# Performance work log

Hardware: AMD Instinct MI355X
Metric: run time of the kernel (lower is better)

## Reference

```python
import jax, jax.numpy as jnp
import numpy as np

B, R, N, F = 16, 13, 392, 256
POOL_CH = 512
NB_CLASSES = 200
ALPHA = 0.5
BN_EPS = 1e-3


def gcn_norm_ones(n):
    # GCNConv.preprocess on an all-ones adjacency: A_hat = A + I, D = (n+1)I,
    # D^-1/2 A_hat D^-1/2 = (ones + eye) / (n + 1)
    return (jnp.ones((n, n), jnp.float32) + jnp.eye(n, dtype=jnp.float32)) / (n + 1.0)


def appnp(x, A, w, b, alpha):
    # Spektral APPNPConv, no hidden layers, mlp_activation='sigmoid', propagations=1
    h = jax.nn.sigmoid(x @ w + b)
    return (1.0 - alpha) * jnp.einsum('mn,...nf->...mf', A, h) + alpha * h


def gat_dense(x, A, kernel, attn_s, attn_n, bias):
    # Faithful translation of the modified GATConv._call_dense
    xk = jnp.einsum('...ni,iho->...nho', x, kernel)            # [..., N, H, Fo]
    s = jnp.einsum('...nhi,iho->...nho', xk, attn_s)           # [..., N, H, 1]
    nb = jnp.einsum('...nhi,iho->...nho', xk, attn_n)          # [..., N, H, 1]
    nb = jnp.einsum('...abc->...cba', nb)                      # [..., 1, H, N]
    coef = jax.nn.leaky_relu(s + nb, 0.2)                      # [..., N, H, N]
    # add_self_loops then mask where a == 0 (normalized ones adjacency -> no masking)
    a = A.at[jnp.arange(A.shape[-1]), jnp.arange(A.shape[-1])].set(1.0)
    mask = jnp.where(a == 0.0, -1e10, 0.0).astype(coef.dtype)  # [N, N]
    coef = coef + mask[:, None, :]
    coef = jax.nn.softmax(coef, axis=-1)
    out = jnp.einsum('...nhm,...mhi->...nhi', coef, xk)        # [..., N, H, Fo]
    out = out.reshape(out.shape[:-2] + (-1,)) + bias           # concat heads
    return jax.nn.elu(out)


def setup_inputs() -> dict:
    key = jax.random.key(0)
    ks = jax.random.split(key, 8)
    s = lambda k, shape, sc: (jax.random.normal(k, shape, jnp.float32) * sc)
    return {
        'x': s(ks[0], (B, R, N, F), 1.0),
        'w_mlp': s(ks[1], (F, F), F ** -0.5),
        'b_mlp': jnp.zeros((F,), jnp.float32),
        'k_gat': s(ks[2], (F, 1, F), F ** -0.5),
        'a_self': s(ks[3], (F, 1, 1), F ** -0.5),
        'a_neigh': s(ks[4], (F, 1, 1), F ** -0.5),
        'b_gat': jnp.zeros((F,), jnp.float32),
        'wf_pool': s(ks[5], (F, POOL_CH), F ** -0.5),
        'bf_pool': jnp.zeros((POOL_CH,), jnp.float32),
        'wa_pool': s(ks[6], (F, POOL_CH), F ** -0.5),
        'ba_pool': jnp.zeros((POOL_CH,), jnp.float32),
        'bn_gamma': jnp.ones((POOL_CH,), jnp.float32),
        'bn_beta': jnp.zeros((POOL_CH,), jnp.float32),
        'bn_mean': jnp.zeros((POOL_CH,), jnp.float32),
        'bn_var': jnp.ones((POOL_CH,), jnp.float32),
        'w_out': s(ks[7], (POOL_CH, NB_CLASSES), POOL_CH ** -0.5),
        'b_out': jnp.zeros((NB_CLASSES,), jnp.float32),
    }


def reference(x, w_mlp, b_mlp, k_gat, a_self, a_neigh, b_gat,
              wf_pool, bf_pool, wa_pool, ba_pool,
              bn_gamma, bn_beta, bn_mean, bn_var, w_out, b_out):
    A_intra = gcn_norm_ones(N)   # [N, N]
    A_inter = gcn_norm_ones(R)   # [R, R]

    # Intra-ROI: APPNP + residual, GAT + residual (all R graphs share weights/adj)
    h = appnp(x, A_intra, w_mlp, b_mlp, ALPHA) + x                      # [B,R,N,F]
    x2_intra = gat_dense(h, A_intra, k_gat, a_self, a_neigh, b_gat) + h
    x2_intra = x2_intra.reshape(x.shape[0], R * N, F)

    # Inter-ROI: transpose so ROIs are the graph nodes
    xt = jnp.transpose(x, (0, 2, 1, 3))                                 # [B,N,R,F]
    h2 = appnp(xt, A_inter, w_mlp, b_mlp, ALPHA) + xt
    x2_inter = gat_dense(h2, A_inter, k_gat, a_self, a_neigh, b_gat) + h2
    x2_inter = x2_inter.reshape(x.shape[0], N * R, F)

    x2 = jnp.concatenate([x2_intra, x2_inter], axis=1)                  # [B, 2RN, F]

    # GlobalAttentionPool(512)
    attn = jax.nn.sigmoid(x2 @ wa_pool + ba_pool)
    feat = x2 @ wf_pool + bf_pool
    pooled = jnp.sum(attn * feat, axis=1)                               # [B, 512]

    # BatchNorm (inference) + softmax classifier
    bn = (pooled - bn_mean) * jax.lax.rsqrt(bn_var + BN_EPS) * bn_gamma + bn_beta
    return jax.nn.softmax(bn @ w_out + b_out, axis=-1)
```

## Files before the change

kernel.cpp:

```cpp
#include <hip/hip_runtime.h>
#include <hip/hip_bf16.h>

#define B_    16
#define R_    13
#define N_    392
#define F_    256
#define RN_   (R_*N_)
#define M_    (B_*RN_)
#define POOL_ 512
#define NCLS_ 200
#define KP_   416
#define WPS_  424

typedef __attribute__((ext_vector_type(4))) float f32x4;
typedef __attribute__((ext_vector_type(8))) short bf16x8;
typedef __attribute__((ext_vector_type(8))) unsigned short u16x8;

__device__ __forceinline__ unsigned short f2b(float f){
  union { float f; unsigned u; } v; v.f = f;
  unsigned r = v.u + 0x7FFF + ((v.u >> 16) & 1);
  return (unsigned short)(r >> 16);
}
__device__ __forceinline__ float b2f(unsigned short b){
  union { unsigned u; float f; } v; v.u = ((unsigned)b) << 16;
  return v.f;
}

__device__ __forceinline__ float warpMax(float v){
  #pragma unroll
  for (int o = 32; o; o >>= 1) v = fmaxf(v, __shfl_down(v, o));
  return v;
}
__device__ __forceinline__ float warpSum(float v){
  #pragma unroll
  for (int o = 32; o; o >>= 1) v += __shfl_down(v, o);
  return v;
}
__device__ __forceinline__ float blockMax(float v, float* red){
  v = warpMax(v);
  __syncthreads();
  if ((threadIdx.x & 63) == 0) red[threadIdx.x >> 6] = v;
  __syncthreads();
  return fmaxf(fmaxf(red[0], red[1]), fmaxf(red[2], red[3]));
}
__device__ __forceinline__ float blockSum(float v, float* red){
  v = warpSum(v);
  __syncthreads();
  if ((threadIdx.x & 63) == 0) red[threadIdx.x >> 6] = v;
  __syncthreads();
  return red[0] + red[1] + red[2] + red[3];
}
__device__ __forceinline__ float eluf(float v){
  return v > 0.f ? v : (expf(v) - 1.f);
}

__global__ __launch_bounds__(256) void cvt_wt(const float* __restrict__ W,
    unsigned short* __restrict__ Wt, int K, int N){
  const int id = blockIdx.x*256 + threadIdx.x;
  if (id < K*N){
    const int n = id / K, k = id - n*K;
    Wt[id] = f2b(W[k*N + n]);
  }
}

__global__ __launch_bounds__(256) void cvt_x(const float* __restrict__ x,
    unsigned short* __restrict__ xb){
  const long t = (long)blockIdx.x*256 + threadIdx.x;
  const float4 a = *(const float4*)&x[t*8];
  const float4 b = *(const float4*)&x[t*8 + 4];
  u16x8 o = {f2b(a.x),f2b(a.y),f2b(a.z),f2b(a.w),f2b(b.x),f2b(b.y),f2b(b.z),f2b(b.w)};
  *(u16x8*)&xb[t*8] = o;
}

__global__ __launch_bounds__(256) void cvt_xT(const float* __restrict__ x,
    unsigned short* __restrict__ xb){
  const long t = (long)blockIdx.x*256 + threadIdx.x;
  const int l  = (int)(t >> 5);
  const int c8 = ((int)t & 31) * 8;
  const int b  = l / RN_;
  const int rem = l - b*RN_;
  const int n  = rem / R_;
  const int r  = rem - n*R_;
  const long prow = (long)(b*R_ + r)*N_ + n;
  const float4 a  = *(const float4*)&x[prow*F_ + c8];
  const float4 bb = *(const float4*)&x[prow*F_ + c8 + 4];
  u16x8 o = {f2b(a.x),f2b(a.y),f2b(a.z),f2b(a.w),f2b(bb.x),f2b(bb.y),f2b(bb.z),f2b(bb.w)};
  *(u16x8*)&xb[(long)l*F_ + c8] = o;
}

template<int ACT>
__global__ __launch_bounds__(256) void mfma_gemm(
    const unsigned short* __restrict__ A, const unsigned short* __restrict__ Wt,
    const float* __restrict__ bias, unsigned short* __restrict__ out){
  __shared__ unsigned short A_lds[128][72];
  __shared__ unsigned short W_lds[64][72];
  const int tid = threadIdx.x;
  const int lane = tid & 63, wid = tid >> 6;
  const int wr = wid >> 1, wc = wid & 1;
  const int lr = lane & 15, lk = lane >> 4;
  const int row0 = blockIdx.x * 128;
  const int col0 = blockIdx.y * 64;

  f32x4 acc[4][2] = {};
  for (int k0 = 0; k0 < 256; k0 += 64){
    #pragma unroll
    for (int i = 0; i < 4; ++i){
      const int chunk = tid + i*256;
      const int r = chunk >> 3, c8 = (chunk & 7)*8;
      *(u16x8*)&A_lds[r][c8] = *(const u16x8*)&A[(long)(row0 + r)*F_ + k0 + c8];
    }
    #pragma unroll
    for (int i = 0; i < 2; ++i){
      const int chunk = tid + i*256;
      const int r = chunk >> 3, c8 = (chunk & 7)*8;
      *(u16x8*)&W_lds[r][c8] = *(const u16x8*)&Wt[(long)(col0 + r)*F_ + k0 + c8];
    }
    __syncthreads();
    #pragma unroll
    for (int kk = 0; kk < 64; kk += 32){
      bf16x8 af[4], bf[2];
      #pragma unroll
      for (int m = 0; m < 4; ++m)
        af[m] = *(const bf16x8*)&A_lds[wr*64 + m*16 + lr][kk + lk*8];
      #pragma unroll
      for (int n = 0; n < 2; ++n)
        bf[n] = *(const bf16x8*)&W_lds[wc*32 + n*16 + lr][kk + lk*8];
      #pragma unroll
      for (int m = 0; m < 4; ++m)
        #pragma unroll
        for (int n = 0; n < 2; ++n)
          acc[m][n] = __builtin_amdgcn_mfma_f32_16x16x32_bf16(af[m], bf[n], acc[m][n], 0, 0, 0);
    }
    __syncthreads();
  }
  #pragma unroll
  for (int m = 0; m < 4; ++m){
    const int gr = row0 + wr*64 + m*16 + lk*4;
    #pragma unroll
    for (int n = 0; n < 2; ++n){
      const int gc = col0 + wc*32 + n*16 + lr;
      #pragma unroll
      for (int q = 0; q < 4; ++q){
        float v = acc[m][n][q];
        if (ACT) v = 1.f/(1.f + expf(-(v + bias[gc])));
        out[(long)(gr + q)*F_ + gc] = f2b(v);
      }
    }
  }
}

__global__ __launch_bounds__(256) void xkT_k(const unsigned short* __restrict__ xk,
    unsigned short* __restrict__ xkT){
  __shared__ unsigned short tile[32][36];
  const int n0 = blockIdx.x * 32;
  const int f0 = blockIdx.y * 32;
  const int g  = blockIdx.z;
  const int t  = threadIdx.x;
  {
    const int nl = t >> 3, fl = (t & 7)*4;
    ushort4 v = {0,0,0,0};
    const int n = n0 + nl;
    if (n < N_) v = *(const ushort4*)&xk[((long)g*N_ + n)*F_ + f0 + fl];
    tile[nl][fl] = v.x; tile[nl][fl+1] = v.y; tile[nl][fl+2] = v.z; tile[nl][fl+3] = v.w;
  }
  __syncthreads();
  {
    const int fl = t >> 3, nl = (t & 7)*4;
    ushort4 o = {tile[nl][fl], tile[nl+1][fl], tile[nl+2][fl], tile[nl+3][fl]};
    *(ushort4*)&xkT[((long)g*F_ + f0 + fl)*KP_ + n0 + nl] = o;
  }
}

__global__ __launch_bounds__(256) void colsum_k(const unsigned short* __restrict__ h1,
    float* __restrict__ S, int nn){
  const int g = blockIdx.x;
  const int f = threadIdx.x;
  const unsigned short* base = h1 + (long)g*nn*F_ + f;
  float s = 0.f;
  for (int n = 0; n < nn; ++n) s += b2f(base[(long)n*F_]);
  S[(long)g*F_ + f] = s;
}

template<int XMODE>
__global__ __launch_bounds__(256) void combine_k(const unsigned short* __restrict__ h1,
    const float* __restrict__ S, const float* __restrict__ x,
    unsigned short* __restrict__ hb){
  const long t = (long)blockIdx.x*256 + threadIdx.x;
  const long row = t >> 6;
  const int f4 = ((int)t & 63) * 4;
  int g, xrow;
  if (XMODE == 0){ g = (int)(row / N_); xrow = (int)row; }
  else {
    g = (int)(row / R_);
    const int b   = (int)(row / RN_);
    const int rem = (int)(row - (long)b*RN_);
    const int n   = rem / R_;
    const int r   = rem - n*R_;
    xrow = (b*R_ + r)*N_ + n;
  }
  const float inv = (XMODE == 0) ? (1.f/(N_+1)) : (1.f/(R_+1));
  const ushort4 hraw = *(const ushort4*)&h1[row*F_ + f4];
  const float4 h1v = {b2f(hraw.x), b2f(hraw.y), b2f(hraw.z), b2f(hraw.w)};
  const float4 Sv  = *(const float4*)&S[(long)g*F_ + f4];
  const float4 xv  = *(const float4*)&x[(long)xrow*F_ + f4];
  float4 o;
  o.x = 0.5f*(Sv.x + h1v.x)*inv + 0.5f*h1v.x + xv.x;
  o.y = 0.5f*(Sv.y + h1v.y)*inv + 0.5f*h1v.y + xv.y;
  o.z = 0.5f*(Sv.z + h1v.z)*inv + 0.5f*h1v.z + xv.z;
  o.w = 0.5f*(Sv.w + h1v.w)*inv + 0.5f*h1v.w + xv.w;
  const ushort4 ob = {f2b(o.x), f2b(o.y), f2b(o.z), f2b(o.w)};
  *(ushort4*)&hb[row*F_ + f4] = ob;
}

__global__ __launch_bounds__(256) void st_k(const unsigned short* __restrict__ xk,
    const float* __restrict__ a_self, const float* __restrict__ a_neigh,
    float* __restrict__ sv, float* __restrict__ tv){
  const int lane = threadIdx.x & 63;
  const int wid  = threadIdx.x >> 6;
  const long row = (long)blockIdx.x*4 + wid;
  const ushort4 raw = *(const ushort4*)&xk[row*F_ + lane*4];
  const float4 v  = {b2f(raw.x), b2f(raw.y), b2f(raw.z), b2f(raw.w)};
  const float4 as = *(const float4*)&a_self[lane*4];
  const float4 an = *(const float4*)&a_neigh[lane*4];
  float s = v.x*as.x + v.y*as.y + v.z*as.z + v.w*as.w;
  float t = v.x*an.x + v.y*an.y + v.z*an.z + v.w*an.w;
  #pragma unroll
  for (int o = 32; o; o >>= 1){ s += __shfl_down(s, o); t += __shfl_down(t, o); }
  if (lane == 0){ sv[row] = s; tv[row] = t; }
}

__global__ __launch_bounds__(256) void attn_intra_k(
    const unsigned short* __restrict__ xkT, const float* __restrict__ sv,
    const float* __restrict__ tv, const float* __restrict__ bg,
    unsigned short* __restrict__ hx2){
  __shared__ unsigned short Wp[64][WPS_];
  __shared__ float t_lds[N_];
  __shared__ float s_lds[64];
  __shared__ float invr[64];
  __shared__ float red[4];
  const int g  = blockIdx.y;
  const int m0 = blockIdx.x * 64;
  const int tid = threadIdx.x;
  const int lane = tid & 63, wid = tid >> 6;

  for (int n = tid; n < N_; n += 256) t_lds[n] = tv[(long)g*N_ + n];
  if (tid < 64) s_lds[tid] = (m0 + tid < N_) ? sv[(long)g*N_ + m0 + tid] : 0.f;
  __syncthreads();
  float tl = -1e30f;
  for (int n = tid; n < N_; n += 256) tl = fmaxf(tl, t_lds[n]);
  const float tmax = blockMax(tl, red);

  for (int j = 0; j < 16; ++j){
    const int row = wid*16 + j;
    const float sm = s_lds[row];
    float zm = sm + tmax; zm = zm > 0.f ? zm : 0.2f*zm;
    float loc = 0.f;
    for (int n = lane; n < KP_; n += 64){
      float e = 0.f;
      if (n < N_){
        float z = sm + t_lds[n];
        z = z > 0.f ? z : 0.2f*z;
        e = expf(z - zm);
        loc += e;
      }
      Wp[row][n] = f2b(e);
    }
    loc = warpSum(loc);
    if (lane == 0) invr[row] = 1.f / loc;
  }
  __syncthreads();

  const int lr = lane & 15, lk = lane >> 4;
  const int c0w = wid * 64;
  const unsigned short* xkTg = xkT + (long)g*F_*KP_;
  f32x4 acc[4][4] = {};
  for (int ks = 0; ks < 13; ++ks){
    const int k0 = ks*32;
    bf16x8 af[4], bfr[4];
    #pragma unroll
    for (int mi = 0; mi < 4; ++mi)
      af[mi] = *(const bf16x8*)&Wp[mi*16 + lr][k0 + lk*8];
    #pragma unroll
    for (int ni = 0; ni < 4; ++ni)
      bfr[ni] = *(const bf16x8*)&xkTg[(long)(c0w + ni*16 + lr)*KP_ + k0 + lk*8];
    #pragma unroll
    for (int mi = 0; mi < 4; ++mi)
      #pragma unroll
      for (int ni = 0; ni < 4; ++ni)
        acc[mi][ni] = __builtin_amdgcn_mfma_f32_16x16x32_bf16(af[mi], bfr[ni], acc[mi][ni], 0, 0, 0);
  }
  #pragma unroll
  for (int mi = 0; mi < 4; ++mi){
    #pragma unroll
    for (int q = 0; q < 4; ++q){
      const int lm = mi*16 + lk*4 + q;
      const int m = m0 + lm;
      if (m < N_){
        const float iv = invr[lm];
        #pragma unroll
        for (int ni = 0; ni < 4; ++ni){
          const int f = c0w + ni*16 + lr;
          const long idx = ((long)g*N_ + m)*F_ + f;
          const float v = eluf(acc[mi][ni][q]*iv + bg[f]) + b2f(hx2[idx]);
          hx2[idx] = f2b(v);
        }
      }
    }
  }
}

__global__ __launch_bounds__(256) void attn_inter_k(
    const unsigned short* __restrict__ xk, const float* __restrict__ sv,
    const float* __restrict__ tv, const float* __restrict__ bg,
    unsigned short* __restrict__ hx2){
  const int g = blockIdx.x;
  const int tid = threadIdx.x;
  __shared__ float w_lds[R_][R_];
  __shared__ float invr[R_];
  __shared__ float st[R_], tt[R_];
  if (tid < R_){ st[tid] = sv[(long)g*R_ + tid]; tt[tid] = tv[(long)g*R_ + tid]; }
  __syncthreads();
  if (tid < R_){
    const float sm = st[tid];
    float z[R_];
    float zm = -1e30f;
    #pragma unroll
    for (int n = 0; n < R_; ++n){
      float zz = sm + tt[n];
      zz = zz > 0.f ? zz : 0.2f*zz;
      z[n] = zz;
      zm = fmaxf(zm, zz);
    }
    float sum = 0.f;
    #pragma unroll
    for (int n = 0; n < R_; ++n){
      const float e = expf(z[n] - zm);
      w_lds[tid][n] = e;
      sum += e;
    }
    invr[tid] = 1.f/sum;
  }
  __syncthreads();
  float acc[R_] = {};
  const unsigned short* xkg = xk + (long)g*R_*F_;
  #pragma unroll
  for (int n = 0; n < R_; ++n){
    const float xv = b2f(xkg[n*F_ + tid]);
    #pragma unroll
    for (int m = 0; m < R_; ++m) acc[m] += w_lds[m][n]*xv;
  }
  const float bgv = bg[tid];
  #pragma unroll
  for (int m = 0; m < R_; ++m){
    const long idx = ((long)g*R_ + m)*F_ + tid;
    const float hv = b2f(hx2[idx]);
    hx2[idx] = f2b(eluf(acc[m]*invr[m] + bgv) + hv);
  }
}

__global__ __launch_bounds__(256) void pool_mfma(
    const unsigned short* __restrict__ x2, const unsigned short* __restrict__ wat,
    const unsigned short* __restrict__ wft, const float* __restrict__ ba,
    const float* __restrict__ bfp, float* __restrict__ pooled){
  __shared__ unsigned short A_lds[128][72];
  __shared__ unsigned short Wa_lds[64][72];
  __shared__ unsigned short Wf_lds[64][72];
  __shared__ float redp[8][64];
  const int tid = threadIdx.x;
  const int lane = tid & 63, wid = tid >> 6;
  const int wr = wid >> 1, wc = wid & 1;
  const int lr = lane & 15, lk = lane >> 4;
  const int j0 = blockIdx.x * 128;
  const int c0 = blockIdx.y * 64;
  const int b  = blockIdx.z;
  const unsigned short* xb = x2 + (long)b * RN_ * F_;

  f32x4 accA[4][2] = {}, accF[4][2] = {};
  for (int k0 = 0; k0 < 256; k0 += 64){
    #pragma unroll
    for (int i = 0; i < 4; ++i){
      const int chunk = tid + i*256;
      const int r = chunk >> 3, c8 = (chunk & 7)*8;
      u16x8 v = {};
      if (j0 + r < RN_) v = *(const u16x8*)&xb[(long)(j0 + r)*F_ + k0 + c8];
      *(u16x8*)&A_lds[r][c8] = v;
    }
    #pragma unroll
    for (int i = 0; i < 2; ++i){
      const int chunk = tid + i*256;
      const int r = chunk >> 3, c8 = (chunk & 7)*8;
      *(u16x8*)&Wa_lds[r][c8] = *(const u16x8*)&wat[(long)(c0 + r)*F_ + k0 + c8];
      *(u16x8*)&Wf_lds[r][c8] = *(const u16x8*)&wft[(long)(c0 + r)*F_ + k0 + c8];
    }
    __syncthreads();
    #pragma unroll
    for (int kk = 0; kk < 64; kk += 32){
      bf16x8 af[4], bfa[2], bff[2];
      #pragma unroll
      for (int m = 0; m < 4; ++m)
        af[m] = *(const bf16x8*)&A_lds[wr*64 + m*16 + lr][kk + lk*8];
      #pragma unroll
      for (int n = 0; n < 2; ++n){
        bfa[n] = *(const bf16x8*)&Wa_lds[wc*32 + n*16 + lr][kk + lk*8];
        bff[n] = *(const bf16x8*)&Wf_lds[wc*32 + n*16 + lr][kk + lk*8];
      }
      #pragma unroll
      for (int m = 0; m < 4; ++m)
        #pragma unroll
        for (int n = 0; n < 2; ++n){
          accA[m][n] = __builtin_amdgcn_mfma_f32_16x16x32_bf16(af[m], bfa[n], accA[m][n], 0, 0, 0);
          accF[m][n] = __builtin_amdgcn_mfma_f32_16x16x32_bf16(af[m], bff[n], accF[m][n], 0, 0, 0);
        }
    }
    __syncthreads();
  }
  float csum[2] = {0.f, 0.f};
  #pragma unroll
  for (int m = 0; m < 4; ++m){
    const int jb = wr*64 + m*16 + lk*4;
    #pragma unroll
    for (int q = 0; q < 4; ++q){
      if (j0 + jb + q < RN_){
        #pragma unroll
        for (int n = 0; n < 2; ++n){
          const int c = c0 + wc*32 + n*16 + lr;
          const float a = accA[m][n][q] + ba[c];
          const float f = accF[m][n][q] + bfp[c];
          csum[n] += f / (1.f + expf(-a));
        }
      }
    }
  }
  #pragma unroll
  for (int n = 0; n < 2; ++n) redp[wr*4 + lk][wc*32 + n*16 + lr] = csum[n];
  __syncthreads();
  if (tid < 64){
    float s = 0.f;
    #pragma unroll
    for (int i = 0; i < 8; ++i) s += redp[i][tid];
    atomicAdd(&pooled[(long)b*POOL_ + c0 + tid], s);
  }
}

__global__ __launch_bounds__(256) void final_k(const float* __restrict__ pooled,
    const float* __restrict__ gamma, const float* __restrict__ beta,
    const float* __restrict__ mean, const float* __restrict__ var,
    const float* __restrict__ wout, const float* __restrict__ bout,
    float* __restrict__ out){
  const int b = blockIdx.x, tid = threadIdx.x;
  __shared__ float bn[POOL_];
  __shared__ float red[4];
  for (int c = tid; c < POOL_; c += 256){
    const float p = pooled[(long)b*POOL_ + c];
    bn[c] = (p - mean[c]) * rsqrtf(var[c] + 1e-3f) * gamma[c] + beta[c];
  }
  __syncthreads();
  float logit = -3.0e38f;
  if (tid < NCLS_){
    float s = bout[tid];
    for (int k = 0; k < POOL_; ++k) s += bn[k]*wout[k*NCLS_ + tid];
    logit = s;
  }
  const float mx = blockMax(logit, red);
  float e = (tid < NCLS_) ? expf(logit - mx) : 0.f;
  const float tot = blockSum(e, red);
  if (tid < NCLS_) out[(long)b*NCLS_ + tid] = e / tot;
}

extern "C" void kernel_launch(void* const* d_in, const int* in_sizes, int n_in,
                              void* d_out, int out_size, void* d_ws, size_t ws_size,
                              hipStream_t stream){
  const float* x       = (const float*)d_in[0];
  const float* w_mlp   = (const float*)d_in[1];
  const float* b_mlp   = (const float*)d_in[2];
  const float* k_gat   = (const float*)d_in[3];
  const float* a_self  = (const float*)d_in[4];
  const float* a_neigh = (const float*)d_in[5];
  const float* b_gat   = (const float*)d_in[6];
  const float* wf_pool = (const float*)d_in[7];
  const float* bf_pool = (const float*)d_in[8];
  const float* wa_pool = (const float*)d_in[9];
  const float* ba_pool = (const float*)d_in[10];
  const float* bn_g    = (const float*)d_in[11];
  const float* bn_b    = (const float*)d_in[12];
  const float* bn_m    = (const float*)d_in[13];
  const float* bn_v    = (const float*)d_in[14];
  const float* w_out   = (const float*)d_in[15];
  const float* b_out   = (const float*)d_in[16];
  float* out = (float*)d_out;

  char* p = (char*)d_ws;
  const long MF = (long)M_ * F_;
  unsigned short* abuf = (unsigned short*)p;  p += MF*2;
  unsigned short* xbuf = (unsigned short*)p;  p += MF*2;
  unsigned short* xkT  = (unsigned short*)p;  p += (long)B_*R_*F_*KP_*2;
  unsigned short* wmt  = (unsigned short*)p;  p += 65536*2;
  unsigned short* kgt  = (unsigned short*)p;  p += 65536*2;
  unsigned short* wat  = (unsigned short*)p;  p += 131072*2;
  unsigned short* wft  = (unsigned short*)p;  p += 131072*2;
  float*          Sbuf = (float*)p;           p += (long)B_*N_*F_*4;
  float*          sbuf = (float*)p;           p += (long)M_*4;
  float*          tbuf = (float*)p;           p += (long)M_*4;
  float*          pooled = (float*)p;         p += (long)B_*POOL_*4;

  hipMemsetAsync(pooled, 0, (size_t)B_*POOL_*sizeof(float), stream);

  cvt_wt<<<256, 256, 0, stream>>>(w_mlp,   wmt, 256, 256);
  cvt_wt<<<256, 256, 0, stream>>>(k_gat,   kgt, 256, 256);
  cvt_wt<<<512, 256, 0, stream>>>(wa_pool, wat, 256, 512);
  cvt_wt<<<512, 256, 0, stream>>>(wf_pool, wft, 256, 512);

  const dim3 ggrid(M_/128, F_/64);
  const dim3 pgrid((RN_+127)/128, POOL_/64, B_);

  cvt_x<<<M_*F_/2048, 256, 0, stream>>>(x, xbuf);
  mfma_gemm<1><<<ggrid, 256, 0, stream>>>(xbuf, wmt, b_mlp, abuf);
  colsum_k<<<B_*R_, 256, 0, stream>>>(abuf, Sbuf, N_);
  combine_k<0><<<M_*64/256, 256, 0, stream>>>(abuf, Sbuf, x, xbuf);
  mfma_gemm<0><<<ggrid, 256, 0, stream>>>(xbuf, kgt, nullptr, abuf);
  xkT_k<<<dim3(KP_/32, F_/32, B_*R_), 256, 0, stream>>>(abuf, xkT);
  st_k<<<M_/4, 256, 0, stream>>>(abuf, a_self, a_neigh, sbuf, tbuf);
  attn_intra_k<<<dim3(7, B_*R_), 256, 0, stream>>>(xkT, sbuf, tbuf, b_gat, xbuf);
  pool_mfma<<<pgrid, 256, 0, stream>>>(xbuf, wat, wft, ba_pool, bf_pool, pooled);

  cvt_xT<<<M_*F_/2048, 256, 0, stream>>>(x, xbuf);
  mfma_gemm<1><<<ggrid, 256, 0, stream>>>(xbuf, wmt, b_mlp, abuf);
  colsum_k<<<B_*N_, 256, 0, stream>>>(abuf, Sbuf, R_);
  combine_k<1><<<M_*64/256, 256, 0, stream>>>(abuf, Sbuf, x, xbuf);
  mfma_gemm<0><<<ggrid, 256, 0, stream>>>(xbuf, kgt, nullptr, abuf);
  st_k<<<M_/4, 256, 0, stream>>>(abuf, a_self, a_neigh, sbuf, tbuf);
  attn_inter_k<<<B_*N_, 256, 0, stream>>>(abuf, sbuf, tbuf, b_gat, xbuf);
  pool_mfma<<<pgrid, 256, 0, stream>>>(xbuf, wat, wft, ba_pool, bf_pool, pooled);

  final_k<<<B_, 256, 0, stream>>>(pooled, bn_g, bn_b, bn_m, bn_v, w_out, b_out, out);
}
```

Measured before the change: 959.5 us.

## Keep attention probabilities in registers and give each wave 16 rows by all columns

The intra-ROI attention kernel no longer writes the softmax weights to a shared-memory tile. Each wave now computes its own 16 rows of bf16 probabilities directly into MFMA A-fragments held in registers, and accumulates all 256 output features for those rows. This removes the LDS staging and its read-back traffic, and frees about 54KB of LDS, which may allow more resident blocks. In exchange, each wave reads the whole xkT B-operand (16 column tiles instead of 4), which raises global/L2 traffic fourfold, and register use rises (13 fragments plus 16 accumulators).

```diff
diff --git a/kernel.cpp b/kernel.cpp
--- a/kernel.cpp
+++ b/kernel.cpp
@@ -10,7 +10,6 @@
 #define POOL_ 512
 #define NCLS_ 200
 #define KP_   416
-#define WPS_  424
 
 typedef __attribute__((ext_vector_type(4))) float f32x4;
 typedef __attribute__((ext_vector_type(8))) short bf16x8;
@@ -233,15 +232,15 @@
     const unsigned short* __restrict__ xkT, const float* __restrict__ sv,
     const float* __restrict__ tv, const float* __restrict__ bg,
     unsigned short* __restrict__ hx2){
-  __shared__ unsigned short Wp[64][WPS_];
   __shared__ float t_lds[N_];
   __shared__ float s_lds[64];
-  __shared__ float invr[64];
+  __shared__ float invr[4][16];
   __shared__ float red[4];
   const int g  = blockIdx.y;
   const int m0 = blockIdx.x * 64;
   const int tid = threadIdx.x;
   const int lane = tid & 63, wid = tid >> 6;
+  const int lr = lane & 15, lk = lane >> 4;
 
   for (int n = tid; n < N_; n += 256) t_lds[n] = tv[(long)g*N_ + n];
   if (tid < 64) s_lds[tid] = (m0 + tid < N_) ? sv[(long)g*N_ + m0 + tid] : 0.f;
@@ -250,60 +249,56 @@
   for (int n = tid; n < N_; n += 256) tl = fmaxf(tl, t_lds[n]);
   const float tmax = blockMax(tl, red);
 
-  for (int j = 0; j < 16; ++j){
-    const int row = wid*16 + j;
-    const float sm = s_lds[row];
-    float zm = sm + tmax; zm = zm > 0.f ? zm : 0.2f*zm;
-    float loc = 0.f;
-    for (int n = lane; n < KP_; n += 64){
+  const float srow = s_lds[wid*16 + lr];
+  float zm = srow + tmax; zm = zm > 0.f ? zm : 0.2f*zm;
+  float lsum = 0.f;
+  bf16x8 pfrag[13];
+  #pragma unroll
+  for (int ks = 0; ks < 13; ++ks){
+    const int base = ks*32 + lk*8;
+    u16x8 pk;
+    #pragma unroll
+    for (int j = 0; j < 8; ++j){
+      const int col = base + j;
       float e = 0.f;
-      if (n < N_){
-        float z = sm + t_lds[n];
+      if (col < N_){
+        float z = srow + t_lds[col];
         z = z > 0.f ? z : 0.2f*z;
         e = expf(z - zm);
-        loc += e;
+        lsum += e;
       }
-      Wp[row][n] = f2b(e);
-    }
-    loc = warpSum(loc);
-    if (lane == 0) invr[row] = 1.f / loc;
-  }
-  __syncthreads();
-
-  const int lr = lane & 15, lk = lane >> 4;
-  const int c0w = wid * 64;
+      pk[j] = f2b(e);
+    }
+    pfrag[ks] = *(bf16x8*)&pk;
+  }
+  lsum += __shfl_xor(lsum, 16);
+  lsum += __shfl_xor(lsum, 32);
+  if (lk == 0) invr[wid][lr] = 1.f / lsum;
+  __syncthreads();
+
   const unsigned short* xkTg = xkT + (long)g*F_*KP_;
-  f32x4 acc[4][4] = {};
+  f32x4 acc[16] = {};
   for (int ks = 0; ks < 13; ++ks){
-    const int k0 = ks*32;
-    bf16x8 af[4], bfr[4];
-    #pragma unroll
-    for (int mi = 0; mi < 4; ++mi)
-      af[mi] = *(const bf16x8*)&Wp[mi*16 + lr][k0 + lk*8];
-    #pragma unroll
-    for (int ni = 0; ni < 4; ++ni)
-      bfr[ni] = *(const bf16x8*)&xkTg[(long)(c0w + ni*16 + lr)*KP_ + k0 + lk*8];
-    #pragma unroll
-    for (int mi = 0; mi < 4; ++mi)
-      #pragma unroll
-      for (int ni = 0; ni < 4; ++ni)
-        acc[mi][ni] = __builtin_amdgcn_mfma_f32_16x16x32_bf16(af[mi], bfr[ni], acc[mi][ni], 0, 0, 0);
-  }
-  #pragma unroll
-  for (int mi = 0; mi < 4; ++mi){
-    #pragma unroll
-    for (int q = 0; q < 4; ++q){
-      const int lm = mi*16 + lk*4 + q;
-      const int m = m0 + lm;
-      if (m < N_){
-        const float iv = invr[lm];
-        #pragma unroll
-        for (int ni = 0; ni < 4; ++ni){
-          const int f = c0w + ni*16 + lr;
-          const long idx = ((long)g*N_ + m)*F_ + f;
-          const float v = eluf(acc[mi][ni][q]*iv + bg[f]) + b2f(hx2[idx]);
-          hx2[idx] = f2b(v);
-        }
+    const int k0 = ks*32 + lk*8;
+    #pragma unroll
+    for (int ni = 0; ni < 16; ++ni){
+      const bf16x8 bfr = *(const bf16x8*)&xkTg[(long)(ni*16 + lr)*KP_ + k0];
+      acc[ni] = __builtin_amdgcn_mfma_f32_16x16x32_bf16(pfrag[ks], bfr, acc[ni], 0, 0, 0);
+    }
+  }
+
+  #pragma unroll
+  for (int q = 0; q < 4; ++q){
+    const int lm = lk*4 + q;
+    const int m = m0 + wid*16 + lm;
+    if (m < N_){
+      const float iv = invr[wid][lm];
+      #pragma unroll
+      for (int ni = 0; ni < 16; ++ni){
+        const int f = ni*16 + lr;
+        const long idx = ((long)g*N_ + m)*F_ + f;
+        const float v = eluf(acc[ni][q]*iv + bg[f]) + b2f(hx2[idx]);
+        hx2[idx] = f2b(v);
       }
     }
   }
```

New measurement: 966.0 us. Within noise of the previous version (+0.7%).
